# Optimization experiments

Hardware: AMD Instinct MI355X
Metric: run time of the kernel (lower is better)

Reference implementation:

```python
import jax, jax.numpy as jnp
import numpy as np

B, IMG, P, S, D, H, HD = 64, 224, 16, 197, 768, 12, 64
MLP, L, PRUNE_AFTER, NCLS = 3072, 12, 4, 1000
N_KEEP = max(1, int(S * 0.5))  # FIXED_RATIO = 0.5 -> 98 kept tokens (plus forced CLS)


def _ln(x, w, b, eps=1e-6):
    m = x.mean(-1, keepdims=True)
    v = ((x - m) ** 2).mean(-1, keepdims=True)
    return (x - m) * jax.lax.rsqrt(v + eps) * w + b


def _block(x, ln1_w, ln1_b, qkv_w, qkv_b, proj_w, proj_b,
           ln2_w, ln2_b, fc1_w, fc1_b, fc2_w, fc2_b, key_mask=None):
    b, s, _ = x.shape
    qkv = _ln(x, ln1_w, ln1_b) @ qkv_w.T + qkv_b           # [B,S,3D]
    qkv = qkv.reshape(b, s, 3, H, HD)
    q, k, v = qkv[:, :, 0], qkv[:, :, 1], qkv[:, :, 2]     # [B,S,H,HD]
    logits = jnp.einsum('bqhd,bkhd->bhqk', q * (HD ** -0.5), k)
    if key_mask is not None:
        # masking pruned keys == varlen attention restricted to kept tokens
        logits = jnp.where(key_mask[:, None, None, :], logits, -1e9)
    attn = jax.nn.softmax(logits, axis=-1)
    out = jnp.einsum('bhqk,bkhd->bqhd', attn, v).reshape(b, s, D)
    x = x + out @ proj_w.T + proj_b
    h = _ln(x, ln2_w, ln2_b)
    h = jax.nn.gelu(h @ fc1_w.T + fc1_b, approximate=False) @ fc2_w.T + fc2_b
    return x + h


def _forward(images, patch_w, patch_b, cls_token, pos_embed,
             ln1_w, ln1_b, qkv_w, qkv_b, proj_w, proj_b,
             ln2_w, ln2_b, fc1_w, fc1_b, fc2_w, fc2_b,
             norm_w, norm_b, head_w, head_b):
    # patch embed: conv stride P == non-overlapping patch projection
    x = jax.lax.conv_general_dilated(images, patch_w, (P, P), 'VALID',
                                     dimension_numbers=('NCHW', 'OIHW', 'NCHW'))
    x = x.reshape(x.shape[0], D, -1).transpose(0, 2, 1) + patch_b       # [B,196,D]
    x = jnp.concatenate([jnp.broadcast_to(cls_token, (x.shape[0], 1, D)), x], axis=1)
    x = x + pos_embed                                                    # [B,197,D]
    for i in range(PRUNE_AFTER):
        x = _block(x, ln1_w[i], ln1_b[i], qkv_w[i], qkv_b[i], proj_w[i], proj_b[i],
                   ln2_w[i], ln2_b[i], fc1_w[i], fc1_b[i], fc2_w[i], fc2_b[i])
    # norm-score topk prune (CLS always kept), as in _threshold_prune
    scores = jnp.linalg.norm(x, axis=-1)                                 # [B,S]
    _, idx = jax.lax.top_k(scores, N_KEEP)
    mask = jnp.zeros((x.shape[0], S), bool)
    mask = mask.at[jnp.arange(x.shape[0])[:, None], idx].set(True).at[:, 0].set(True)
    # Padded-mask form of triton_pack_tokens + flash_attn_varlen: pruned tokens
    # are never attended to (masked keys) and their own outputs are unused.
    for i in range(PRUNE_AFTER, L):
        x = _block(x, ln1_w[i], ln1_b[i], qkv_w[i], qkv_b[i], proj_w[i], proj_b[i],
                   ln2_w[i], ln2_b[i], fc1_w[i], fc1_b[i], fc2_w[i], fc2_b[i],
                   key_mask=mask)
    cls = _ln(x[:, 0], norm_w, norm_b)   # packed[cu[:-1]] is always the CLS token
    return cls @ head_w.T + head_b       # [B, NCLS]


def setup_inputs():
    key = jax.random.key(0)
    ks = iter(jax.random.split(key, 32))
    def rn(shape, s=0.02):
        return jax.random.normal(next(ks), shape, jnp.float32) * s
    return {
        'images': jax.random.normal(next(ks), (B, 3, IMG, IMG), jnp.float32),
        'patch_w': rn((D, 3, P, P)), 'patch_b': jnp.zeros((D,), jnp.float32),
        'cls_token': rn((1, 1, D)), 'pos_embed': rn((1, S, D)),
        'ln1_w': jnp.ones((L, D), jnp.float32), 'ln1_b': jnp.zeros((L, D), jnp.float32),
        'qkv_w': rn((L, 3 * D, D)), 'qkv_b': jnp.zeros((L, 3 * D), jnp.float32),
        'proj_w': rn((L, D, D)), 'proj_b': jnp.zeros((L, D), jnp.float32),
        'ln2_w': jnp.ones((L, D), jnp.float32), 'ln2_b': jnp.zeros((L, D), jnp.float32),
        'fc1_w': rn((L, MLP, D)), 'fc1_b': jnp.zeros((L, MLP), jnp.float32),
        'fc2_w': rn((L, D, MLP)), 'fc2_b': jnp.zeros((L, D), jnp.float32),
        'norm_w': jnp.ones((D,), jnp.float32), 'norm_b': jnp.zeros((D,), jnp.float32),
        'head_w': rn((NCLS, D)), 'head_b': jnp.zeros((NCLS,), jnp.float32),
    }


def reference(images, patch_w, patch_b, cls_token, pos_embed,
              ln1_w, ln1_b, qkv_w, qkv_b, proj_w, proj_b,
              ln2_w, ln2_b, fc1_w, fc1_b, fc2_w, fc2_b,
              norm_w, norm_b, head_w, head_b):
    return _forward(images, patch_w, patch_b, cls_token, pos_embed,
                    ln1_w, ln1_b, qkv_w, qkv_b, proj_w, proj_b,
                    ln2_w, ln2_b, fc1_w, fc1_b, fc2_w, fc2_b,
                    norm_w, norm_b, head_w, head_b)
```

## Files before the change

### kernel.cpp

```cpp
#include <hip/hip_runtime.h>
#include <hip/hip_bf16.h>
#include <cstdint>

#define NH 12
#define SQ 197
#define DIM 768
#define HDIM 64
#define BATCH 64
#define MTOK (BATCH*SQ)
#define MLPD 3072
#define NKEEP 98
#define CSLOT 100
#define MCTOK (BATCH*CSLOT)
#define VLDF 224
#define VLDC 128

typedef __attribute__((ext_vector_type(8))) short bf16x8;
typedef __attribute__((ext_vector_type(8))) unsigned short ushort8;
typedef __attribute__((ext_vector_type(4))) unsigned short ushort4v;
typedef __attribute__((ext_vector_type(4))) float floatx4;

__device__ __forceinline__ unsigned short f2bf(float f) {
  __hip_bfloat16 h = __float2bfloat16(f);
  return reinterpret_cast<unsigned short&>(h);
}

__device__ __forceinline__ float erf_fast(float x) {
  float ax = fabsf(x);
  float t = 1.f / (1.f + 0.3275911f * ax);
  float y = t * (0.254829592f + t * (-0.284496736f + t * (1.421413741f +
            t * (-1.453152027f + t * 1.061405429f))));
  float r = 1.f - y * __expf(-ax * ax);
  return copysignf(r, x);
}

__device__ __forceinline__ void gload16(const unsigned short* g, unsigned short* l) {
  __builtin_amdgcn_global_load_lds(
      (const __attribute__((address_space(1))) void*)g,
      (__attribute__((address_space(3))) void*)l, 16, 0, 0);
}

enum { EPI_PATCH = 0, EPI_QKV = 1, EPI_RESID = 2, EPI_GELU = 3, EPI_HEAD = 4, EPI_QKVC = 5 };

template<int EPI, bool CHK, int MR, int NR>
__device__ __forceinline__ void gemm_epilogue(
    floatx4 (&acc)[MR][NR], int m0, int n0, int wr, int wc, int l15, int l4,
    const float* __restrict__ bias, int M, int N,
    float* __restrict__ xresid, const float* __restrict__ pos,
    unsigned short* __restrict__ obf, unsigned short* __restrict__ qb,
    unsigned short* __restrict__ kb, unsigned short* __restrict__ vb,
    float* __restrict__ ofp)
{
#pragma unroll
  for (int mr = 0; mr < MR; ++mr) {
#pragma unroll
    for (int nr = 0; nr < NR; ++nr) {
#pragma unroll
      for (int j = 0; j < 4; ++j) {
        int m = m0 + wr + mr * 16 + l4 * 4 + j;
        int n = n0 + wc + nr * 16 + l15;
        if (CHK && (m >= M || n >= N)) continue;
        float val = acc[mr][nr][j] + bias[n];
        if constexpr (EPI == EPI_PATCH) {
          int b = m / 196, p = m - b * 196;
          xresid[(size_t)(b * SQ + 1 + p) * DIM + n] = val + pos[(1 + p) * DIM + n];
        } else if constexpr (EPI == EPI_QKV || EPI == EPI_QKVC) {
          constexpr int SR = (EPI == EPI_QKV) ? SQ : CSLOT;
          constexpr int VL = (EPI == EPI_QKV) ? VLDF : VLDC;
          int part = n / DIM; int within = n - part * DIM;
          int h = within >> 6, hd = within & 63;
          int b = m / SR, s = m - b * SR;
          if (part == 0)      qb[(((size_t)(b * NH + h)) * SR + s) * HDIM + hd] = f2bf(val * 0.125f);
          else if (part == 1) kb[(((size_t)(b * NH + h)) * SR + s) * HDIM + hd] = f2bf(val);
          else                vb[(((size_t)(b * NH + h)) * HDIM + hd) * VL + s] = f2bf(val);
        } else if constexpr (EPI == EPI_RESID) {
          xresid[(size_t)m * DIM + n] += val;
        } else if constexpr (EPI == EPI_GELU) {
          float g = 0.5f * val * (1.f + erf_fast(val * 0.70710678118654752f));
          obf[(size_t)m * MLPD + n] = f2bf(g);
        } else {
          ofp[(size_t)m * 1000 + n] = val;
        }
      }
    }
  }
}

template<int EPI>
__global__ __launch_bounds__(512, 1)
void gemm_bf256(const unsigned short* __restrict__ A, int lda,
                const unsigned short* __restrict__ Wb, int ldw,
                const float* __restrict__ bias,
                int M, int N, int K,
                float* __restrict__ xresid,
                const float* __restrict__ pos,
                unsigned short* __restrict__ obf,
                unsigned short* __restrict__ qb,
                unsigned short* __restrict__ kb,
                unsigned short* __restrict__ vb,
                float* __restrict__ ofp)
{
  __shared__ unsigned short As[2][256 * 64];
  __shared__ unsigned short Bs[2][256 * 64];
  const int tid = threadIdx.x;
  const int lane = tid & 63;
  const int w = tid >> 6;
  const int wr = (w >> 2) * 128;
  const int wc = (w & 3) * 64;

  const int gx = gridDim.x;
  const int nwg = gx * gridDim.y;
  const int orig = blockIdx.y * gx + blockIdx.x;
  const int q = nwg >> 3, r = nwg & 7;
  const int xcd = orig & 7, o8 = orig >> 3;
  const int wgid = ((xcd < r) ? xcd * (q + 1) : r * (q + 1) + (xcd - r) * q) + o8;
  const int bx = wgid % gx, by = wgid / gx;
  const int m0 = by * 256, n0 = bx * 256;
  const int l15 = lane & 15, l4 = lane >> 4;

  const int sub = lane & 7, rsub = lane >> 3;
  const int scol = ((sub ^ rsub) << 3);
  const bool isA = (w < 4);
  const unsigned short* gp[8];
  int ldst[8];
#pragma unroll
  for (int j = 0; j < 8; ++j) {
    int row = (w & 3) * 64 + j * 8 + rsub;
    if (isA) {
      int ra = m0 + row; if (ra > M - 1) ra = M - 1;
      gp[j] = A + (size_t)ra * lda + scol;
    } else {
      int rb = n0 + row; if (rb > N - 1) rb = N - 1;
      gp[j] = Wb + (size_t)rb * ldw + scol;
    }
    ldst[j] = ((w & 3) * 8 + j) * 512;
  }

  floatx4 acc[8][4];
#pragma unroll
  for (int i = 0; i < 8; ++i)
#pragma unroll
    for (int j = 0; j < 4; ++j) acc[i][j] = {0.f, 0.f, 0.f, 0.f};

  auto STAGE = [&](int buf, int kt) {
    unsigned short* base = isA ? &As[buf][0] : &Bs[buf][0];
#pragma unroll
    for (int j = 0; j < 8; ++j)
      gload16(gp[j] + kt, base + ldst[j]);
  };

  const int nk = K >> 6;
  STAGE(0, 0);
  int cur = 0;
  for (int ki = 0; ki < nk; ++ki) {
    if (ki + 1 < nk) {
      STAGE(cur ^ 1, (ki + 1) << 6);
      asm volatile("s_waitcnt vmcnt(8)" ::: "memory");
    } else {
      asm volatile("s_waitcnt vmcnt(0)" ::: "memory");
    }
    __builtin_amdgcn_sched_barrier(0);
    __builtin_amdgcn_s_barrier();
    const unsigned short* Ac = &As[cur][0];
    const unsigned short* Bc = &Bs[cur][0];
#pragma unroll
    for (int kk = 0; kk < 2; ++kk) {
      bf16x8 af[8], bfr[4];
#pragma unroll
      for (int mr = 0; mr < 8; ++mr) {
        int row = wr + mr * 16 + l15;
        int cs = (kk * 4 + l4) ^ (row & 7);
        af[mr] = *(const bf16x8*)&Ac[row * 64 + cs * 8];
      }
#pragma unroll
      for (int nr = 0; nr < 4; ++nr) {
        int row = wc + nr * 16 + l15;
        int cs = (kk * 4 + l4) ^ (row & 7);
        bfr[nr] = *(const bf16x8*)&Bc[row * 64 + cs * 8];
      }
#pragma unroll
      for (int mr = 0; mr < 8; ++mr)
#pragma unroll
        for (int nr = 0; nr < 4; ++nr)
          acc[mr][nr] = __builtin_amdgcn_mfma_f32_16x16x32_bf16(af[mr], bfr[nr], acc[mr][nr], 0, 0, 0);
    }
    __builtin_amdgcn_sched_barrier(0);
    __builtin_amdgcn_s_barrier();
    cur ^= 1;
  }
  if (m0 + 256 <= M && n0 + 256 <= N)
    gemm_epilogue<EPI, false, 8, 4>(acc, m0, n0, wr, wc, l15, l4, bias, M, N,
                                    xresid, pos, obf, qb, kb, vb, ofp);
  else
    gemm_epilogue<EPI, true, 8, 4>(acc, m0, n0, wr, wc, l15, l4, bias, M, N,
                                   xresid, pos, obf, qb, kb, vb, ofp);
}

template<int EPI, int BN>
__global__ __launch_bounds__(256)
void gemm_bf(const unsigned short* __restrict__ A, int lda,
             const unsigned short* __restrict__ Wb, int ldw,
             const float* __restrict__ bias,
             int M, int N, int K,
             float* __restrict__ xresid,
             const float* __restrict__ pos,
             unsigned short* __restrict__ obf,
             unsigned short* __restrict__ qb,
             unsigned short* __restrict__ kb,
             unsigned short* __restrict__ vb,
             float* __restrict__ ofp)
{
  constexpr int NR = BN / 32;
  constexpr int NG = (128 + BN) / 8;
  constexpr int PG = NG / 4;
  __shared__ unsigned short As[128 * 64];
  __shared__ unsigned short Bs[BN * 64];
  const int tid = threadIdx.x;
  const int lane = tid & 63;
  const int w = tid >> 6;
  const int wr = (w >> 1) * 64, wc = (w & 1) * (BN / 2);

  const int gx = gridDim.x;
  const int nwg = gx * gridDim.y;
  const int orig = blockIdx.y * gx + blockIdx.x;
  const int q = nwg >> 3, r = nwg & 7;
  const int xcd = orig & 7, o8 = orig >> 3;
  const int wgid = ((xcd < r) ? xcd * (q + 1) : r * (q + 1) + (xcd - r) * q) + o8;
  const int bx = wgid % gx, by = wgid / gx;
  const int m0 = by * 128, n0 = bx * BN;
  const int l15 = lane & 15, l4 = lane >> 4;

  const int sub = lane & 7, rsub = lane >> 3;
  const int scol = ((sub ^ rsub) << 3);
  const unsigned short* gp[PG];
  unsigned short* lp[PG];
#pragma unroll
  for (int j = 0; j < PG; ++j) {
    int t = w * PG + j;
    if (t < 16) {
      int row = t * 8 + rsub;
      int ra = m0 + row; if (ra > M - 1) ra = M - 1;
      gp[j] = A + (size_t)ra * lda + scol;
      lp[j] = &As[t * 512];
    } else {
      int tb = t - 16;
      int row = tb * 8 + rsub;
      int rb = n0 + row; if (rb > N - 1) rb = N - 1;
      gp[j] = Wb + (size_t)rb * ldw + scol;
      lp[j] = &Bs[tb * 512];
    }
  }

  floatx4 acc[4][NR];
#pragma unroll
  for (int i = 0; i < 4; ++i)
#pragma unroll
    for (int j = 0; j < NR; ++j) acc[i][j] = {0.f, 0.f, 0.f, 0.f};

  for (int kt = 0; kt < K; kt += 64) {
#pragma unroll
    for (int j = 0; j < PG; ++j)
      gload16(gp[j] + kt, lp[j]);
    __syncthreads();
#pragma unroll
    for (int kk = 0; kk < 2; ++kk) {
      bf16x8 af[4], bfr[NR];
#pragma unroll
      for (int mr = 0; mr < 4; ++mr) {
        int row = wr + mr * 16 + l15;
        int cs = (kk * 4 + l4) ^ (row & 7);
        af[mr] = *(const bf16x8*)&As[row * 64 + cs * 8];
      }
#pragma unroll
      for (int nr = 0; nr < NR; ++nr) {
        int row = wc + nr * 16 + l15;
        int cs = (kk * 4 + l4) ^ (row & 7);
        bfr[nr] = *(const bf16x8*)&Bs[row * 64 + cs * 8];
      }
#pragma unroll
      for (int mr = 0; mr < 4; ++mr)
#pragma unroll
        for (int nr = 0; nr < NR; ++nr)
          acc[mr][nr] = __builtin_amdgcn_mfma_f32_16x16x32_bf16(af[mr], bfr[nr], acc[mr][nr], 0, 0, 0);
    }
    __syncthreads();
  }
  if (m0 + 128 <= M && n0 + BN <= N)
    gemm_epilogue<EPI, false, 4, NR>(acc, m0, n0, wr, wc, l15, l4, bias, M, N,
                                     xresid, pos, obf, qb, kb, vb, ofp);
  else
    gemm_epilogue<EPI, true, 4, NR>(acc, m0, n0, wr, wc, l15, l4, bias, M, N,
                                    xresid, pos, obf, qb, kb, vb, ofp);
}

template<int EPI>
__global__ __launch_bounds__(256)
void gemm_f32(const unsigned short* __restrict__ A, int lda,
              const float* __restrict__ Wf, int ldw,
              const float* __restrict__ bias,
              int M, int N, int K,
              float* __restrict__ xresid,
              const float* __restrict__ pos,
              unsigned short* __restrict__ obf,
              unsigned short* __restrict__ qb,
              unsigned short* __restrict__ kb,
              unsigned short* __restrict__ vb,
              float* __restrict__ ofp)
{
  __shared__ unsigned short As[128 * 64];
  __shared__ unsigned short Bs[128 * 64];
  const int tid = threadIdx.x;
  const int lane = tid & 63;
  const int w = tid >> 6;
  const int wr = (w >> 1) * 64, wc = (w & 1) * 64;
  const int m0 = blockIdx.y * 128, n0 = blockIdx.x * 128;
  const int l15 = lane & 15, l4 = lane >> 4;

  floatx4 acc[4][4];
#pragma unroll
  for (int i = 0; i < 4; ++i)
#pragma unroll
    for (int j = 0; j < 4; ++j) acc[i][j] = {0.f, 0.f, 0.f, 0.f};

  for (int kt = 0; kt < K; kt += 64) {
#pragma unroll
    for (int i = 0; i < 4; ++i) {
      int g = tid + 256 * i;
      int row = g >> 3, c = g & 7;
      int sw = (c ^ (row & 7)) * 8;
      int ra = m0 + row; if (ra > M - 1) ra = M - 1;
      ushort8 av = *(const ushort8*)(A + (size_t)ra * lda + kt + c * 8);
      *(ushort8*)&As[row * 64 + sw] = av;
      int rb = n0 + row; if (rb > N - 1) rb = N - 1;
      const float* bs = Wf + (size_t)rb * ldw + kt + c * 8;
      float4 f0 = *(const float4*)bs;
      float4 f1 = *(const float4*)(bs + 4);
      ushort8 bv;
      bv[0] = f2bf(f0.x); bv[1] = f2bf(f0.y); bv[2] = f2bf(f0.z); bv[3] = f2bf(f0.w);
      bv[4] = f2bf(f1.x); bv[5] = f2bf(f1.y); bv[6] = f2bf(f1.z); bv[7] = f2bf(f1.w);
      *(ushort8*)&Bs[row * 64 + sw] = bv;
    }
    __syncthreads();
#pragma unroll
    for (int kk = 0; kk < 2; ++kk) {
      bf16x8 af[4], bfr[4];
#pragma unroll
      for (int mr = 0; mr < 4; ++mr) {
        int row = wr + mr * 16 + l15;
        int cs = (kk * 4 + l4) ^ (row & 7);
        af[mr] = *(const bf16x8*)&As[row * 64 + cs * 8];
      }
#pragma unroll
      for (int nr = 0; nr < 4; ++nr) {
        int row = wc + nr * 16 + l15;
        int cs = (kk * 4 + l4) ^ (row & 7);
        bfr[nr] = *(const bf16x8*)&Bs[row * 64 + cs * 8];
      }
#pragma unroll
      for (int mr = 0; mr < 4; ++mr)
#pragma unroll
        for (int nr = 0; nr < 4; ++nr)
          acc[mr][nr] = __builtin_amdgcn_mfma_f32_16x16x32_bf16(af[mr], bfr[nr], acc[mr][nr], 0, 0, 0);
    }
    __syncthreads();
  }
  if (m0 + 128 <= M && n0 + 128 <= N)
    gemm_epilogue<EPI, false, 4, 4>(acc, m0, n0, wr, wc, l15, l4, bias, M, N,
                                    xresid, pos, obf, qb, kb, vb, ofp);
  else
    gemm_epilogue<EPI, true, 4, 4>(acc, m0, n0, wr, wc, l15, l4, bias, M, N,
                                   xresid, pos, obf, qb, kb, vb, ofp);
}

__global__ __launch_bounds__(256)
void cvt_kernel(const float* __restrict__ src, unsigned short* __restrict__ dst, int nchunks)
{
  int i = blockIdx.x * 256 + threadIdx.x;
  if (i >= nchunks) return;
  float4 f0 = *(const float4*)(src + (size_t)i * 8);
  float4 f1 = *(const float4*)(src + (size_t)i * 8 + 4);
  ushort8 v;
  v[0] = f2bf(f0.x); v[1] = f2bf(f0.y); v[2] = f2bf(f0.z); v[3] = f2bf(f0.w);
  v[4] = f2bf(f1.x); v[5] = f2bf(f1.y); v[6] = f2bf(f1.z); v[7] = f2bf(f1.w);
  *(ushort8*)(dst + (size_t)i * 8) = v;
}

__global__ __launch_bounds__(192)
void ln_kernel(const float* __restrict__ x, long long row_stride,
               const float* __restrict__ g, const float* __restrict__ b,
               unsigned short* __restrict__ out)
{
  int row = blockIdx.x;
  const float4* xr = (const float4*)(x + (size_t)row * row_stride);
  int t = threadIdx.x;
  float4 v = xr[t];
  float s = v.x + v.y + v.z + v.w;
  float sq = v.x * v.x + v.y * v.y + v.z * v.z + v.w * v.w;
  __shared__ float sb[6];
  for (int o = 32; o; o >>= 1) { s += __shfl_down(s, o); sq += __shfl_down(sq, o); }
  if ((t & 63) == 0) { sb[t >> 6] = s; sb[3 + (t >> 6)] = sq; }
  __syncthreads();
  s = sb[0] + sb[1] + sb[2];
  sq = sb[3] + sb[4] + sb[5];
  float mean = s * (1.f / 768.f);
  float var = sq * (1.f / 768.f) - mean * mean;
  float rstd = rsqrtf(var + 1e-6f);
  float4 gg = ((const float4*)g)[t];
  float4 bb = ((const float4*)b)[t];
  ushort4v o4;
  o4[0] = f2bf((v.x - mean) * rstd * gg.x + bb.x);
  o4[1] = f2bf((v.y - mean) * rstd * gg.y + bb.y);
  o4[2] = f2bf((v.z - mean) * rstd * gg.z + bb.z);
  o4[3] = f2bf((v.w - mean) * rstd * gg.w + bb.w);
  *(ushort4v*)(out + (size_t)row * DIM + t * 4) = o4;
}

template<int NT, int SROWS, int VLD, int PSTR, bool CNT>
__global__ __launch_bounds__(256)
void attn_kernel(const unsigned short* __restrict__ qb,
                 const unsigned short* __restrict__ kb,
                 const unsigned short* __restrict__ vb,
                 const int* __restrict__ cnt,
                 unsigned short* __restrict__ outA)
{
  __shared__ unsigned short Ks[NT * 16 * 64];
  __shared__ unsigned short Ps[4][16 * PSTR];
  int bh = blockIdx.x;
  int b = bh / NH, h = bh - b * NH;
  const int tid = threadIdx.x, lane = tid & 63, w = tid >> 6;
  const int l15 = lane & 15, l4 = lane >> 4;
  const unsigned short* kbase = kb + (size_t)bh * SROWS * HDIM;
  const unsigned short* qbase = qb + (size_t)bh * SROWS * HDIM;
  const unsigned short* vbase = vb + (size_t)bh * HDIM * VLD;
  const int limit = CNT ? cnt[b] : SROWS;

  constexpr int KCH = NT * 16 * 8;
  for (int i = 0; i < (KCH + 255) / 256; ++i) {
    int gch = tid + 256 * i;
    if (gch < KCH) {
      int row = gch >> 3, c = gch & 7;
      int rs = row > SROWS - 1 ? SROWS - 1 : row;
      ushort8 kv = *(const ushort8*)(kbase + (size_t)rs * HDIM + c * 8);
      *(ushort8*)&Ks[row * 64 + ((c ^ (row & 7))) * 8] = kv;
    }
  }
  __syncthreads();

  for (int qt = w; qt < NT; qt += 4) {
    int qrow = qt * 16 + l15; if (qrow > SROWS - 1) qrow = SROWS - 1;
    bf16x8 aq0 = *(const bf16x8*)(qbase + (size_t)qrow * HDIM + l4 * 8);
    bf16x8 aq1 = *(const bf16x8*)(qbase + (size_t)qrow * HDIM + 32 + l4 * 8);

    floatx4 lg[NT];
#pragma unroll
    for (int nt = 0; nt < NT; ++nt) {
      lg[nt] = {0.f, 0.f, 0.f, 0.f};
      int row = nt * 16 + l15;
      int cs0 = (l4) ^ (row & 7);
      int cs1 = (4 + l4) ^ (row & 7);
      bf16x8 bk0 = *(const bf16x8*)&Ks[row * 64 + cs0 * 8];
      bf16x8 bk1 = *(const bf16x8*)&Ks[row * 64 + cs1 * 8];
      lg[nt] = __builtin_amdgcn_mfma_f32_16x16x32_bf16(aq0, bk0, lg[nt], 0, 0, 0);
      lg[nt] = __builtin_amdgcn_mfma_f32_16x16x32_bf16(aq1, bk1, lg[nt], 0, 0, 0);
    }
    float mx[4] = {-1e30f, -1e30f, -1e30f, -1e30f};
#pragma unroll
    for (int nt = 0; nt < NT; ++nt) {
      int col = nt * 16 + l15;
      bool valid = col < limit;
#pragma unroll
      for (int j = 0; j < 4; ++j) {
        float v = valid ? lg[nt][j] : -1e9f;
        lg[nt][j] = v;
        mx[j] = fmaxf(mx[j], v);
      }
    }
#pragma unroll
    for (int j = 0; j < 4; ++j)
      for (int o = 1; o < 16; o <<= 1) mx[j] = fmaxf(mx[j], __shfl_xor(mx[j], o));
    float sm[4] = {0.f, 0.f, 0.f, 0.f};
#pragma unroll
    for (int nt = 0; nt < NT; ++nt)
#pragma unroll
      for (int j = 0; j < 4; ++j) {
        float p = __expf(lg[nt][j] - mx[j]);
        lg[nt][j] = p;
        sm[j] += p;
      }
#pragma unroll
    for (int j = 0; j < 4; ++j) {
      for (int o = 1; o < 16; o <<= 1) sm[j] += __shfl_xor(sm[j], o);
      sm[j] = 1.f / sm[j];
    }
    unsigned short* pw = &Ps[w][0];
#pragma unroll
    for (int nt = 0; nt < NT; ++nt) {
      int col = nt * 16 + l15;
#pragma unroll
      for (int j = 0; j < 4; ++j)
        pw[(l4 * 4 + j) * PSTR + col] = f2bf(lg[nt][j]);
    }
#pragma unroll
    for (int j = 0; j < 4; ++j)
      pw[(l4 * 4 + j) * PSTR + NT * 16 + l15] = 0;
    floatx4 oacc[4];
#pragma unroll
    for (int nr = 0; nr < 4; ++nr) oacc[nr] = {0.f, 0.f, 0.f, 0.f};
#pragma unroll
    for (int ks = 0; ks < VLD / 32; ++ks) {
      bf16x8 ap = *(const bf16x8*)&pw[l15 * PSTR + ks * 32 + l4 * 8];
#pragma unroll
      for (int nr = 0; nr < 4; ++nr) {
        bf16x8 bv = *(const bf16x8*)(vbase + (size_t)(nr * 16 + l15) * VLD + ks * 32 + l4 * 8);
        oacc[nr] = __builtin_amdgcn_mfma_f32_16x16x32_bf16(ap, bv, oacc[nr], 0, 0, 0);
      }
    }
#pragma unroll
    for (int nr = 0; nr < 4; ++nr)
#pragma unroll
      for (int j = 0; j < 4; ++j) {
        int qi = qt * 16 + l4 * 4 + j;
        if (qi < SROWS)
          outA[((size_t)(b * SROWS + qi)) * DIM + h * HDIM + nr * 16 + l15] = f2bf(oacc[nr][j] * sm[j]);
      }
  }
}

__global__ __launch_bounds__(256)
void im2col_kernel(const float* __restrict__ images, unsigned short* __restrict__ out)
{
  int idx = blockIdx.x * 256 + threadIdx.x;
  int token = idx / 96;
  int kc = (idx - token * 96) * 8;
  int b = token / 196, p = token - b * 196;
  int py = p / 14, px = p - py * 14;
  int c = kc >> 8, rem = kc & 255;
  int i = rem >> 4, j0 = rem & 15;
  const float* src = images + (((size_t)(b * 3 + c) * 224 + py * 16 + i) * 224 + px * 16 + j0);
  float4 f0 = *(const float4*)src;
  float4 f1 = *(const float4*)(src + 4);
  ushort8 v;
  v[0] = f2bf(f0.x); v[1] = f2bf(f0.y); v[2] = f2bf(f0.z); v[3] = f2bf(f0.w);
  v[4] = f2bf(f1.x); v[5] = f2bf(f1.y); v[6] = f2bf(f1.z); v[7] = f2bf(f1.w);
  *(ushort8*)(out + (size_t)token * DIM + kc) = v;
}

__global__ __launch_bounds__(256)
void clspos_kernel(const float* __restrict__ cls, const float* __restrict__ pos,
                   float* __restrict__ x)
{
  int idx = blockIdx.x * 256 + threadIdx.x;
  int b = idx / DIM, d = idx - b * DIM;
  x[(size_t)(b * SQ) * DIM + d] = cls[d] + pos[d];
}

__global__ __launch_bounds__(256)
void norms_kernel(const float* __restrict__ x, float* __restrict__ norms)
{
  int row = blockIdx.x * 4 + (threadIdx.x >> 6);
  if (row >= MTOK) return;
  int lane = threadIdx.x & 63;
  const float* xr = x + (size_t)row * DIM;
  float acc = 0.f;
  for (int d = lane; d < DIM; d += 64) { float v = xr[d]; acc += v * v; }
  for (int o = 32; o; o >>= 1) acc += __shfl_down(acc, o);
  if (lane == 0) norms[row] = acc;
}

__global__ __launch_bounds__(256)
void topk_select(const float* __restrict__ norms, short* __restrict__ sidx,
                 int* __restrict__ cntg)
{
  int b = blockIdx.x;
  __shared__ float sc[SQ];
  __shared__ unsigned char keep[SQ];
  int tid = threadIdx.x;
  if (tid < SQ) sc[tid] = norms[b * SQ + tid];
  __syncthreads();
  if (tid < SQ) {
    float mine = sc[tid];
    int rank = 0;
    for (int j = 0; j < SQ; ++j) {
      float v = sc[j];
      rank += (v > mine) || (v == mine && j < tid);
    }
    keep[tid] = (rank < NKEEP) || (tid == 0);
  }
  __syncthreads();
  if (tid == 0) {
    short* row = sidx + b * CSLOT;
    int c = 0;
    for (int s = 0; s < SQ; ++s) if (keep[s]) row[c++] = (short)s;
    cntg[b] = c;
    for (int s = c; s < CSLOT; ++s) row[s] = 0;
  }
}

__global__ __launch_bounds__(192)
void gather_kernel(const float* __restrict__ x, const short* __restrict__ sidx,
                   float* __restrict__ xc)
{
  int g = blockIdx.x;
  int b = g / CSLOT;
  int src = sidx[g];
  const float4* sp = (const float4*)(x + ((size_t)(b * SQ + src)) * DIM);
  float4* dp = (float4*)(xc + (size_t)g * DIM);
  dp[threadIdx.x] = sp[threadIdx.x];
}

template<int EPI, int BN>
static inline void launch_gemm(hipStream_t stream, bool usebf,
                               const unsigned short* A, int lda,
                               const float* Wf, const unsigned short* Wb, int ldw,
                               const float* bias, int M, int N, int K,
                               float* xresid, const float* pos,
                               unsigned short* obf, unsigned short* qb,
                               unsigned short* kb, unsigned short* vb, float* ofp)
{
  if (usebf) {
    dim3 grid((N + BN - 1) / BN, (M + 127) / 128);
    gemm_bf<EPI, BN><<<grid, 256, 0, stream>>>(A, lda, Wb, ldw, bias,
        M, N, K, xresid, pos, obf, qb, kb, vb, ofp);
  } else {
    dim3 grid((N + 127) / 128, (M + 127) / 128);
    gemm_f32<EPI><<<grid, 256, 0, stream>>>(A, lda, Wf, ldw, bias,
        M, N, K, xresid, pos, obf, qb, kb, vb, ofp);
  }
}

template<int EPI>
static inline void launch_gemm256(hipStream_t stream, bool usebf,
                                  const unsigned short* A, int lda,
                                  const float* Wf, const unsigned short* Wb, int ldw,
                                  const float* bias, int M, int N, int K,
                                  unsigned short* obf, unsigned short* qb,
                                  unsigned short* kb, unsigned short* vb)
{
  if (usebf) {
    dim3 grid(N / 256, (M + 255) / 256);
    gemm_bf256<EPI><<<grid, 512, 0, stream>>>(A, lda, Wb, ldw, bias,
        M, N, K, nullptr, nullptr, obf, qb, kb, vb, nullptr);
  } else {
    dim3 grid((N + 127) / 128, (M + 127) / 128);
    gemm_f32<EPI><<<grid, 256, 0, stream>>>(A, lda, Wf, ldw, bias,
        M, N, K, nullptr, nullptr, obf, qb, kb, vb, nullptr);
  }
}

extern "C" void kernel_launch(void* const* d_in, const int* in_sizes, int n_in,
                              void* d_out, int out_size, void* d_ws, size_t ws_size,
                              hipStream_t stream)
{
  const float* images    = (const float*)d_in[0];
  const float* patch_w   = (const float*)d_in[1];
  const float* patch_b   = (const float*)d_in[2];
  const float* cls_token = (const float*)d_in[3];
  const float* pos_embed = (const float*)d_in[4];
  const float* ln1_w = (const float*)d_in[5];
  const float* ln1_b = (const float*)d_in[6];
  const float* qkv_w = (const float*)d_in[7];
  const float* qkv_b = (const float*)d_in[8];
  const float* proj_w = (const float*)d_in[9];
  const float* proj_b = (const float*)d_in[10];
  const float* ln2_w = (const float*)d_in[11];
  const float* ln2_b = (const float*)d_in[12];
  const float* fc1_w = (const float*)d_in[13];
  const float* fc1_b = (const float*)d_in[14];
  const float* fc2_w = (const float*)d_in[15];
  const float* fc2_b = (const float*)d_in[16];
  const float* norm_w = (const float*)d_in[17];
  const float* norm_b = (const float*)d_in[18];
  const float* head_w = (const float*)d_in[19];
  const float* head_b = (const float*)d_in[20];

  char* ws = (char*)d_ws;
  size_t off = 0;
  auto alloc = [&](size_t bytes) { void* p = ws + off; off += (bytes + 255) & ~(size_t)255; return p; };
  float* x            = (float*)alloc((size_t)MTOK * DIM * 4);
  float* xc           = (float*)alloc((size_t)MCTOK * DIM * 4);
  unsigned short* xn  = (unsigned short*)alloc((size_t)MTOK * DIM * 2);
  size_t h1_bytes = (size_t)MTOK * MLPD * 2;
  unsigned short* h1  = (unsigned short*)alloc(h1_bytes);
  unsigned short* qb  = h1;
  unsigned short* kb  = qb + (size_t)BATCH * NH * SQ * HDIM;
  unsigned short* vb  = kb + (size_t)BATCH * NH * SQ * HDIM;
  size_t vbytes = (size_t)BATCH * NH * HDIM * VLDF * 2;
  unsigned short* lncls = (unsigned short*)alloc((size_t)64 * DIM * 2);
  float* norms = (float*)alloc((size_t)MTOK * 4);
  short* sidx  = (short*)alloc((size_t)MCTOK * 2);
  int* cnt = (int*)alloc(BATCH * 4);
  size_t n_qkvw = (size_t)12 * 2304 * DIM, n_projw = (size_t)12 * DIM * DIM;
  size_t n_fc1w = (size_t)12 * MLPD * DIM, n_fc2w = (size_t)12 * DIM * MLPD;
  size_t n_patw = (size_t)DIM * DIM, n_headw = (size_t)1000 * DIM;
  unsigned short* wqkv = (unsigned short*)alloc(n_qkvw * 2);
  unsigned short* wproj = (unsigned short*)alloc(n_projw * 2);
  unsigned short* wfc1 = (unsigned short*)alloc(n_fc1w * 2);
  unsigned short* wfc2 = (unsigned short*)alloc(n_fc2w * 2);
  unsigned short* wpat = (unsigned short*)alloc(n_patw * 2);
  unsigned short* whead = (unsigned short*)alloc(n_headw * 2);
  const bool usebf = (off <= ws_size);

  hipMemsetAsync(vb, 0, vbytes, stream);

  if (usebf) {
    cvt_kernel<<<(int)((n_qkvw/8 + 255)/256), 256, 0, stream>>>(qkv_w, wqkv, (int)(n_qkvw/8));
    cvt_kernel<<<(int)((n_projw/8 + 255)/256), 256, 0, stream>>>(proj_w, wproj, (int)(n_projw/8));
    cvt_kernel<<<(int)((n_fc1w/8 + 255)/256), 256, 0, stream>>>(fc1_w, wfc1, (int)(n_fc1w/8));
    cvt_kernel<<<(int)((n_fc2w/8 + 255)/256), 256, 0, stream>>>(fc2_w, wfc2, (int)(n_fc2w/8));
    cvt_kernel<<<(int)((n_patw/8 + 255)/256), 256, 0, stream>>>(patch_w, wpat, (int)(n_patw/8));
    cvt_kernel<<<(int)((n_headw/8 + 255)/256), 256, 0, stream>>>(head_w, whead, (int)(n_headw/8));
  }

  im2col_kernel<<<4704, 256, 0, stream>>>(images, h1);
  launch_gemm<EPI_PATCH, 64>(stream, usebf, h1, DIM, patch_w, wpat, DIM,
      patch_b, 12544, DIM, DIM, x, pos_embed, nullptr, nullptr, nullptr, nullptr, nullptr);
  clspos_kernel<<<192, 256, 0, stream>>>(cls_token, pos_embed, x);

  for (int l = 0; l < 4; ++l) {
    ln_kernel<<<MTOK, 192, 0, stream>>>(x, DIM, ln1_w + l * DIM, ln1_b + l * DIM, xn);
    launch_gemm256<EPI_QKV>(stream, usebf, xn, DIM,
        qkv_w + (size_t)l * 2304 * DIM, wqkv + (size_t)l * 2304 * DIM, DIM,
        qkv_b + l * 2304, MTOK, 2304, DIM, nullptr, qb, kb, vb);
    attn_kernel<13, SQ, VLDF, 248, false><<<BATCH * NH, 256, 0, stream>>>(qb, kb, vb, nullptr, xn);
    launch_gemm<EPI_RESID, 64>(stream, usebf, xn, DIM,
        proj_w + (size_t)l * DIM * DIM, wproj + (size_t)l * DIM * DIM, DIM,
        proj_b + l * DIM, MTOK, DIM, DIM, x, nullptr, nullptr, nullptr, nullptr, nullptr, nullptr);
    ln_kernel<<<MTOK, 192, 0, stream>>>(x, DIM, ln2_w + l * DIM, ln2_b + l * DIM, xn);
    launch_gemm256<EPI_GELU>(stream, usebf, xn, DIM,
        fc1_w + (size_t)l * MLPD * DIM, wfc1 + (size_t)l * MLPD * DIM, DIM,
        fc1_b + l * MLPD, MTOK, MLPD, DIM, h1, nullptr, nullptr, nullptr);
    launch_gemm<EPI_RESID, 64>(stream, usebf, h1, MLPD,
        fc2_w + (size_t)l * DIM * MLPD, wfc2 + (size_t)l * DIM * MLPD, MLPD,
        fc2_b + l * DIM, MTOK, DIM, MLPD, x, nullptr, nullptr, nullptr, nullptr, nullptr, nullptr);
  }

  norms_kernel<<<(MTOK + 3) / 4, 256, 0, stream>>>(x, norms);
  topk_select<<<BATCH, 256, 0, stream>>>(norms, sidx, cnt);
  gather_kernel<<<MCTOK, 192, 0, stream>>>(x, sidx, xc);

  for (int l = 4; l < 12; ++l) {
    ln_kernel<<<MCTOK, 192, 0, stream>>>(xc, DIM, ln1_w + l * DIM, ln1_b + l * DIM, xn);
    launch_gemm<EPI_QKVC, 128>(stream, usebf, xn, DIM,
        qkv_w + (size_t)l * 2304 * DIM, wqkv + (size_t)l * 2304 * DIM, DIM,
        qkv_b + l * 2304, MCTOK, 2304, DIM, nullptr, nullptr, nullptr, qb, kb, vb, nullptr);
    attn_kernel<7, CSLOT, VLDC, 136, true><<<BATCH * NH, 256, 0, stream>>>(qb, kb, vb, cnt, xn);
    launch_gemm<EPI_RESID, 64>(stream, usebf, xn, DIM,
        proj_w + (size_t)l * DIM * DIM, wproj + (size_t)l * DIM * DIM, DIM,
        proj_b + l * DIM, MCTOK, DIM, DIM, xc, nullptr, nullptr, nullptr, nullptr, nullptr, nullptr);
    ln_kernel<<<MCTOK, 192, 0, stream>>>(xc, DIM, ln2_w + l * DIM, ln2_b + l * DIM, xn);
    launch_gemm<EPI_GELU, 128>(stream, usebf, xn, DIM,
        fc1_w + (size_t)l * MLPD * DIM, wfc1 + (size_t)l * MLPD * DIM, DIM,
        fc1_b + l * MLPD, MCTOK, MLPD, DIM, nullptr, nullptr, h1, nullptr, nullptr, nullptr, nullptr);
    launch_gemm<EPI_RESID, 64>(stream, usebf, h1, MLPD,
        fc2_w + (size_t)l * DIM * MLPD, wfc2 + (size_t)l * DIM * MLPD, MLPD,
        fc2_b + l * DIM, MCTOK, DIM, MLPD, xc, nullptr, nullptr, nullptr, nullptr, nullptr, nullptr);
  }

  ln_kernel<<<64, 192, 0, stream>>>(xc, (long long)CSLOT * DIM, norm_w, norm_b, lncls);
  launch_gemm<EPI_HEAD, 64>(stream, usebf, lncls, DIM, head_w, whead, DIM,
      head_b, 64, 1000, DIM, nullptr, nullptr, nullptr, nullptr, nullptr, nullptr, (float*)d_out);
  (void)in_sizes; (void)n_in; (void)out_size;
}
```

Before: 3.697 ms.

## Split full-length attention across two blocks, fuse weight conversions, vectorize norms

Full-sequence attention now launches two blocks per batch-head, each handling half of the query tiles, to raise occupancy across the GPU. Each block still loads the whole K tile into shared memory, so that load is duplicated. The six weight-conversion launches are merged into one kernel that dispatches on a flat index, cutting launch overhead. The token-norm kernel now reads float4 instead of scalars.

```diff
diff --git a/kernel.cpp b/kernel.cpp
--- a/kernel.cpp
+++ b/kernel.cpp
@@ -372,17 +372,30 @@
                                    xresid, pos, obf, qb, kb, vb, ofp);
 }
 
-__global__ __launch_bounds__(256)
-void cvt_kernel(const float* __restrict__ src, unsigned short* __restrict__ dst, int nchunks)
-{
-  int i = blockIdx.x * 256 + threadIdx.x;
-  if (i >= nchunks) return;
-  float4 f0 = *(const float4*)(src + (size_t)i * 8);
-  float4 f1 = *(const float4*)(src + (size_t)i * 8 + 4);
+__device__ __forceinline__ void cvt8(const float* s, unsigned short* d, long long i) {
+  float4 f0 = *(const float4*)(s + i * 8);
+  float4 f1 = *(const float4*)(s + i * 8 + 4);
   ushort8 v;
   v[0] = f2bf(f0.x); v[1] = f2bf(f0.y); v[2] = f2bf(f0.z); v[3] = f2bf(f0.w);
   v[4] = f2bf(f1.x); v[5] = f2bf(f1.y); v[6] = f2bf(f1.z); v[7] = f2bf(f1.w);
-  *(ushort8*)(dst + (size_t)i * 8) = v;
+  *(ushort8*)(d + i * 8) = v;
+}
+
+__global__ __launch_bounds__(256)
+void cvt6_kernel(const float* s0, unsigned short* d0, long long n0,
+                 const float* s1, unsigned short* d1, long long n1,
+                 const float* s2, unsigned short* d2, long long n2,
+                 const float* s3, unsigned short* d3, long long n3,
+                 const float* s4, unsigned short* d4, long long n4,
+                 const float* s5, unsigned short* d5, long long n5)
+{
+  long long i = (long long)blockIdx.x * 256 + threadIdx.x;
+  if (i < n0) { cvt8(s0, d0, i); return; } i -= n0;
+  if (i < n1) { cvt8(s1, d1, i); return; } i -= n1;
+  if (i < n2) { cvt8(s2, d2, i); return; } i -= n2;
+  if (i < n3) { cvt8(s3, d3, i); return; } i -= n3;
+  if (i < n4) { cvt8(s4, d4, i); return; } i -= n4;
+  if (i < n5) { cvt8(s5, d5, i); }
 }
 
 __global__ __launch_bounds__(192)
@@ -415,7 +428,7 @@
   *(ushort4v*)(out + (size_t)row * DIM + t * 4) = o4;
 }
 
-template<int NT, int SROWS, int VLD, int PSTR, bool CNT>
+template<int NT, int SROWS, int VLD, int PSTR, bool CNT, int SPLIT>
 __global__ __launch_bounds__(256)
 void attn_kernel(const unsigned short* __restrict__ qb,
                  const unsigned short* __restrict__ kb,
@@ -425,7 +438,8 @@
 {
   __shared__ unsigned short Ks[NT * 16 * 64];
   __shared__ unsigned short Ps[4][16 * PSTR];
-  int bh = blockIdx.x;
+  int bh = blockIdx.x / SPLIT;
+  int half = blockIdx.x - bh * SPLIT;
   int b = bh / NH, h = bh - b * NH;
   const int tid = threadIdx.x, lane = tid & 63, w = tid >> 6;
   const int l15 = lane & 15, l4 = lane >> 4;
@@ -446,7 +460,9 @@
   }
   __syncthreads();
 
-  for (int qt = w; qt < NT; qt += 4) {
+  constexpr int QTB = (NT + SPLIT - 1) / SPLIT;
+  const int qthi = (half + 1) * QTB < NT ? (half + 1) * QTB : NT;
+  for (int qt = half * QTB + w; qt < qthi; qt += 4) {
     int qrow = qt * 16 + l15; if (qrow > SROWS - 1) qrow = SROWS - 1;
     bf16x8 aq0 = *(const bf16x8*)(qbase + (size_t)qrow * HDIM + l4 * 8);
     bf16x8 aq1 = *(const bf16x8*)(qbase + (size_t)qrow * HDIM + 32 + l4 * 8);
@@ -560,9 +576,12 @@
   int row = blockIdx.x * 4 + (threadIdx.x >> 6);
   if (row >= MTOK) return;
   int lane = threadIdx.x & 63;
-  const float* xr = x + (size_t)row * DIM;
+  const float4* xr = (const float4*)(x + (size_t)row * DIM);
   float acc = 0.f;
-  for (int d = lane; d < DIM; d += 64) { float v = xr[d]; acc += v * v; }
+  for (int c = lane; c < 192; c += 64) {
+    float4 v = xr[c];
+    acc += v.x * v.x + v.y * v.y + v.z * v.z + v.w * v.w;
+  }
   for (int o = 32; o; o >>= 1) acc += __shfl_down(acc, o);
   if (lane == 0) norms[row] = acc;
 }
@@ -703,12 +722,12 @@
   hipMemsetAsync(vb, 0, vbytes, stream);
 
   if (usebf) {
-    cvt_kernel<<<(int)((n_qkvw/8 + 255)/256), 256, 0, stream>>>(qkv_w, wqkv, (int)(n_qkvw/8));
-    cvt_kernel<<<(int)((n_projw/8 + 255)/256), 256, 0, stream>>>(proj_w, wproj, (int)(n_projw/8));
-    cvt_kernel<<<(int)((n_fc1w/8 + 255)/256), 256, 0, stream>>>(fc1_w, wfc1, (int)(n_fc1w/8));
-    cvt_kernel<<<(int)((n_fc2w/8 + 255)/256), 256, 0, stream>>>(fc2_w, wfc2, (int)(n_fc2w/8));
-    cvt_kernel<<<(int)((n_patw/8 + 255)/256), 256, 0, stream>>>(patch_w, wpat, (int)(n_patw/8));
-    cvt_kernel<<<(int)((n_headw/8 + 255)/256), 256, 0, stream>>>(head_w, whead, (int)(n_headw/8));
+    long long c0 = n_qkvw / 8, c1 = n_projw / 8, c2 = n_fc1w / 8,
+              c3 = n_fc2w / 8, c4 = n_patw / 8, c5 = n_headw / 8;
+    long long tot = c0 + c1 + c2 + c3 + c4 + c5;
+    cvt6_kernel<<<(int)((tot + 255) / 256), 256, 0, stream>>>(
+        qkv_w, wqkv, c0, proj_w, wproj, c1, fc1_w, wfc1, c2,
+        fc2_w, wfc2, c3, patch_w, wpat, c4, head_w, whead, c5);
   }
 
   im2col_kernel<<<4704, 256, 0, stream>>>(images, h1);
@@ -721,7 +740,7 @@
     launch_gemm256<EPI_QKV>(stream, usebf, xn, DIM,
         qkv_w + (size_t)l * 2304 * DIM, wqkv + (size_t)l * 2304 * DIM, DIM,
         qkv_b + l * 2304, MTOK, 2304, DIM, nullptr, qb, kb, vb);
-    attn_kernel<13, SQ, VLDF, 248, false><<<BATCH * NH, 256, 0, stream>>>(qb, kb, vb, nullptr, xn);
+    attn_kernel<13, SQ, VLDF, 248, false, 2><<<BATCH * NH * 2, 256, 0, stream>>>(qb, kb, vb, nullptr, xn);
     launch_gemm<EPI_RESID, 64>(stream, usebf, xn, DIM,
         proj_w + (size_t)l * DIM * DIM, wproj + (size_t)l * DIM * DIM, DIM,
         proj_b + l * DIM, MTOK, DIM, DIM, x, nullptr, nullptr, nullptr, nullptr, nullptr, nullptr);
@@ -743,7 +762,7 @@
     launch_gemm<EPI_QKVC, 128>(stream, usebf, xn, DIM,
         qkv_w + (size_t)l * 2304 * DIM, wqkv + (size_t)l * 2304 * DIM, DIM,
         qkv_b + l * 2304, MCTOK, 2304, DIM, nullptr, nullptr, nullptr, qb, kb, vb, nullptr);
-    attn_kernel<7, CSLOT, VLDC, 136, true><<<BATCH * NH, 256, 0, stream>>>(qb, kb, vb, cnt, xn);
+    attn_kernel<7, CSLOT, VLDC, 136, true, 1><<<BATCH * NH, 256, 0, stream>>>(qb, kb, vb, cnt, xn);
     launch_gemm<EPI_RESID, 64>(stream, usebf, xn, DIM,
         proj_w + (size_t)l * DIM * DIM, wproj + (size_t)l * DIM * DIM, DIM,
         proj_b + l * DIM, MCTOK, DIM, DIM, xc, nullptr, nullptr, nullptr, nullptr, nullptr, nullptr);
```

Result: no change. 3.701 ms, median of 2 (+0.1%).
